# Kernel optimization log

Hardware: AMD Instinct MI355X
Metric: run time of the kernel (lower is better)

The kernel has to match this reference:

```python
import jax, jax.numpy as jnp
import numpy as np

NUM_HEADS = 12

def setup_inputs() -> dict:
    key = jax.random.key(0)
    ks = jax.random.split(key, 6)
    B, N, C, P = 16, 785, 768, 48
    return {
        "x": jax.random.normal(ks[0], (B, N, C), jnp.float32),
        "qkv_w": jax.random.normal(ks[1], (3 * C, C), jnp.float32) * 0.02,
        "pos_emb": jax.random.normal(ks[2], (N, N, P), jnp.float32) * 0.02,
        "pos_proj_w": jax.random.normal(ks[3], (NUM_HEADS, P), jnp.float32) * 0.02,
        "proj_w": jax.random.normal(ks[4], (C, C), jnp.float32) * 0.02,
        "proj_b": jnp.zeros((C,), jnp.float32),
    }

def reference(x, qkv_w, pos_emb, pos_proj_w, proj_w, proj_b):
    B, N, C = x.shape
    H = NUM_HEADS
    hd = C // H
    scale = hd ** -0.5
    # qkv projection: [B,N,3C] -> q,k,v each [B,H,N,hd]
    qkv = (x @ qkv_w.T).reshape(B, N, 3, H, hd)
    qkv = jnp.transpose(qkv, (2, 0, 3, 1, 4))
    q, k, v = qkv[0], qkv[1], qkv[2]
    # learned relative-position bias: [H,N,N]
    pos_score = jnp.einsum('nmp,hp->hnm', pos_emb, pos_proj_w)
    # attention scores: scale applied AFTER adding bias (matches original)
    attn = (jnp.einsum('bhnd,bhmd->bhnm', q, k) + pos_score[None]) * scale
    attn = jax.nn.softmax(attn, axis=-1)
    out = jnp.einsum('bhnm,bhmd->bhnd', attn, v)
    out = jnp.transpose(out, (0, 2, 1, 3)).reshape(B, N, C)
    return out @ proj_w.T + proj_b
```

## Files before the change

kernel.cpp:

```cpp
#include <hip/hip_runtime.h>
#include <hip/hip_fp16.h>

#define B_ 16
#define N_ 785
#define NP 800
#define C_ 768
#define H_ 12
#define HD_ 64
#define P_ 48
#define M_ (B_*N_)
#define MP_ (B_*NP)
#define POSW 832
#define VTW  832
#define SLOG2E 0.1803368801111244f

#define OFF_Q   0
#define OFF_K   9646080
#define OFF_VT  19292160
#define OFF_POS 29515776
#define OFF_XF  37353216
#define OFF_AO  OFF_XF
#define OFF_WQ  47085312
#define OFF_WP  48854784

struct __align__(16) Half8 { __half h[8]; };
typedef _Float16 half8_t __attribute__((ext_vector_type(8)));
typedef _Float16 half4_t __attribute__((ext_vector_type(4)));
typedef float f32x4 __attribute__((ext_vector_type(4)));

__device__ __forceinline__ void gl16(const void* g, void* l) {
    __builtin_amdgcn_global_load_lds(
        (const __attribute__((address_space(1))) void*)g,
        (__attribute__((address_space(3))) void*)l, 16, 0, 0);
}

__device__ __forceinline__ int xcd_swz(int o, int nwg) {
    const int q = nwg >> 3, r = nwg & 7;
    const int xcd = o & 7, idx = o >> 3;
    const int base = xcd < r ? xcd * (q + 1) : r * (q + 1) + (xcd - r) * q;
    return base + idx;
}

#define NX4 2411520
#define NQ4 442368
#define NP4 147456
#define NTOT4 (NX4+NQ4+NP4)

__global__ __launch_bounds__(256) void convert_f16(
    const float* __restrict__ x, const float* __restrict__ wq,
    const float* __restrict__ wp, _Float16* __restrict__ xo,
    _Float16* __restrict__ wqo, _Float16* __restrict__ wpo)
{
    int i = blockIdx.x * 256 + threadIdx.x;
    const float4* s; _Float16* d; int o;
    if (i < NX4)            { s = (const float4*)x;  d = xo;  o = i; }
    else if (i < NX4 + NQ4) { s = (const float4*)wq; d = wqo; o = i - NX4; }
    else                    { s = (const float4*)wp; d = wpo; o = i - NX4 - NQ4; }
    float4 v = s[o];
    half4_t h = { (_Float16)v.x, (_Float16)v.y, (_Float16)v.z, (_Float16)v.w };
    *(half4_t*)&d[o * 4] = h;
}

#define QKV_NWG (18 * 100)

__global__ __launch_bounds__(256) void qkv_gemm_mfma(
    const _Float16* __restrict__ A, const _Float16* __restrict__ Bw,
    _Float16* __restrict__ qh, _Float16* __restrict__ kh, _Float16* __restrict__ vth)
{
    __shared__ _Float16 Asl[2][128 * 32];
    __shared__ _Float16 Bsl[2][128 * 32];

    const int t  = threadIdx.x;
    const int w  = t >> 6;
    const int l  = t & 63;
    const int lr = l & 15;
    const int lg = l >> 4;
    const int wm = (w >> 1) * 64;
    const int wn = (w & 1) * 64;

    const int g   = xcd_swz(blockIdx.x, QKV_NWG);
    const int nt  = g % 18;
    const int n0  = nt * 128;
    const int mp0 = (g / 18) * 128;
    const int tsel  = nt / 6;
    const bool isV  = (tsel == 2);
    const int nbase = n0 - tsel * 768;

    const int f1 = t + 256;
    const int ar0 = t >> 2,  ac0 = (t & 3) * 8;
    const int ar1 = f1 >> 2, ac1 = (f1 & 3) * 8;
    const int mpa = mp0 + ar0, mpb = mp0 + ar1;
    const int xra = (mpa / NP) * N_ + min(mpa % NP, N_ - 1);
    const int xrb = (mpb / NP) * N_ + min(mpb % NP, N_ - 1);
    const _Float16* Ag0 = A  + (size_t)xra * 768 + ac0;
    const _Float16* Ag1 = A  + (size_t)xrb * 768 + ac1;
    const _Float16* Bg0 = Bw + (size_t)(n0 + ar0) * 768 + ac0;
    const _Float16* Bg1 = Bw + (size_t)(n0 + ar1) * 768 + ac1;

    f32x4 acc[4][4];
    #pragma unroll
    for (int i = 0; i < 4; ++i)
        #pragma unroll
        for (int j = 0; j < 4; ++j) acc[i][j] = (f32x4){0.f, 0.f, 0.f, 0.f};

    gl16(Ag0, &Asl[0][t * 8]); gl16(Ag1, &Asl[0][f1 * 8]);
    gl16(Bg0, &Bsl[0][t * 8]); gl16(Bg1, &Bsl[0][f1 * 8]);
    __syncthreads();

    #pragma unroll 2
    for (int it = 0; it < 24; ++it) {
        const int cur = it & 1;
        if (it < 23) {
            const int kn = (it + 1) * 32;
            gl16(Ag0 + kn, &Asl[cur ^ 1][t * 8]); gl16(Ag1 + kn, &Asl[cur ^ 1][f1 * 8]);
            gl16(Bg0 + kn, &Bsl[cur ^ 1][t * 8]); gl16(Bg1 + kn, &Bsl[cur ^ 1][f1 * 8]);
        }
        half8_t af[4], bf[4];
        #pragma unroll
        for (int i = 0; i < 4; ++i)
            af[i] = *(const half8_t*)&Asl[cur][(wm + i * 16 + lr) * 32 + lg * 8];
        #pragma unroll
        for (int j = 0; j < 4; ++j)
            bf[j] = *(const half8_t*)&Bsl[cur][(wn + j * 16 + lr) * 32 + lg * 8];
        __builtin_amdgcn_s_setprio(1);
        if (!isV) {
            #pragma unroll
            for (int i = 0; i < 4; ++i)
                #pragma unroll
                for (int j = 0; j < 4; ++j)
                    acc[i][j] = __builtin_amdgcn_mfma_f32_16x16x32_f16(bf[j], af[i], acc[i][j], 0, 0, 0);
        } else {
            #pragma unroll
            for (int i = 0; i < 4; ++i)
                #pragma unroll
                for (int j = 0; j < 4; ++j)
                    acc[i][j] = __builtin_amdgcn_mfma_f32_16x16x32_f16(af[i], bf[j], acc[i][j], 0, 0, 0);
        }
        __builtin_amdgcn_s_setprio(0);
        __syncthreads();
    }

    if (!isV) {
        _Float16* dstb = (tsel == 0) ? qh : kh;
        const float sc  = (tsel == 0) ? SLOG2E : 1.0f;
        #pragma unroll
        for (int i = 0; i < 4; ++i) {
            const int mp = mp0 + wm + i * 16 + lr;
            const int bb = mp / NP;
            const int nn = mp - bb * NP;
            if (nn >= N_) continue;
            #pragma unroll
            for (int j = 0; j < 4; ++j) {
                const int nq = nbase + wn + j * 16 + lg * 4;
                const int hh = nq >> 6, dd = nq & 63;
                half4_t hv = { (_Float16)(acc[i][j][0] * sc), (_Float16)(acc[i][j][1] * sc),
                               (_Float16)(acc[i][j][2] * sc), (_Float16)(acc[i][j][3] * sc) };
                *(half4_t*)(dstb + ((size_t)(bb * H_ + hh) * N_ + nn) * HD_ + dd) = hv;
            }
        }
    } else {
        #pragma unroll
        for (int i = 0; i < 4; ++i) {
            const int mq  = mp0 + wm + i * 16 + lg * 4;
            const int bb  = mq / NP;
            const int nn0 = mq - bb * NP;
            if (nn0 >= N_) continue;
            const bool full = (nn0 + 3) < N_;
            #pragma unroll
            for (int j = 0; j < 4; ++j) {
                const int n  = nbase + wn + j * 16 + lr;
                const int hh = n >> 6, dd = n & 63;
                _Float16* vb = vth + ((size_t)(bb * H_ + hh) * HD_ + dd) * VTW;
                if (full) {
                    half4_t hv = { (_Float16)acc[i][j][0], (_Float16)acc[i][j][1],
                                   (_Float16)acc[i][j][2], (_Float16)acc[i][j][3] };
                    *(half4_t*)(vb + nn0) = hv;
                } else {
                    #pragma unroll
                    for (int r = 0; r < 4; ++r)
                        if (nn0 + r < N_) vb[nn0 + r] = (_Float16)acc[i][j][r];
                }
            }
        }
    }
}

__global__ __launch_bounds__(256) void pos_kernel(
    const float* __restrict__ pe, const float* __restrict__ pw,
    __half* __restrict__ posh)
{
    __shared__ float W[H_][P_];
    const int t = threadIdx.x;
    for (int i = t; i < H_ * P_; i += 256) W[i / P_][i % P_] = pw[i];
    __syncthreads();
    int nm = blockIdx.x * 256 + t;
    if (nm >= N_ * N_) return;
    float e[48];
    const float4* src = (const float4*)(pe + (size_t)nm * 48);
    #pragma unroll
    for (int i = 0; i < 12; ++i) {
        float4 v = src[i];
        e[4*i] = v.x; e[4*i+1] = v.y; e[4*i+2] = v.z; e[4*i+3] = v.w;
    }
    int n = nm / N_, m = nm - n * N_;
    #pragma unroll
    for (int hh = 0; hh < H_; ++hh) {
        float s = 0.f;
        #pragma unroll
        for (int p = 0; p < 48; ++p) s = fmaf(e[p], W[hh][p], s);
        posh[((size_t)hh * N_ + n) * POSW + m] = __float2half(s * SLOG2E);
    }
}

#define NQT 13
#define ATT_NWG (192 * NQT)

__global__ __launch_bounds__(256) void attn_mfma(
    const _Float16* __restrict__ qh, const _Float16* __restrict__ kh,
    const _Float16* __restrict__ vt, const _Float16* __restrict__ posh,
    _Float16* __restrict__ aoh)
{
    __shared__ _Float16 Kl[2][64][72];
    __shared__ _Float16 Vl[2][64][72];

    const int t  = threadIdx.x;
    const int l  = t & 63;
    const int w  = t >> 6;
    const int lr = l & 15;
    const int lg = l >> 4;

    const int g2   = xcd_swz(blockIdx.x, ATT_NWG);
    const int qt   = g2 % NQT;
    const int rest = g2 / NQT;
    const int b    = rest & 15;
    const int h    = rest >> 4;
    const int bh   = b * H_ + h;
    const int n0   = qt * 64;

    const int qrow = n0 + w * 16 + lr;
    const int qrc  = qrow < N_ ? qrow : N_ - 1;
    const _Float16* qbase = qh + ((size_t)bh * N_ + qrc) * HD_;
    const half8_t qf0 = *(const half8_t*)(qbase + lg * 8);
    const half8_t qf1 = *(const half8_t*)(qbase + 32 + lg * 8);

    f32x4 O0 = {0.f,0.f,0.f,0.f}, O1 = O0, O2 = O0, O3 = O0;
    f32x4 lacc = {0.f,0.f,0.f,0.f};
    float m_run = -1e30f;

    const half8_t vones = { (_Float16)1.f, (_Float16)1.f, (_Float16)1.f, (_Float16)1.f,
                            (_Float16)1.f, (_Float16)1.f, (_Float16)1.f, (_Float16)1.f };

    const int srow = t >> 2;
    const int scol = (t & 3) * 16;
    const int vbase = (scol & 32) + ((scol & 16) >> 2);
    const _Float16* kRow = kh + ((size_t)bh * N_) * HD_ + scol;
    const _Float16* vRow = vt + ((size_t)bh * HD_ + srow) * VTW + scol;
    const _Float16* bFrag = posh + ((size_t)h * N_ + qrc) * POSW + lg * 4;

    half8_t rk0, rk1, rv0, rv1;
    half4_t rbc[4], rbn[4];
    {
        const int gm = srow < N_ ? srow : N_ - 1;
        const half8_t* ks = (const half8_t*)(kRow + (size_t)gm * HD_);
        rk0 = ks[0]; rk1 = ks[1];
        const half8_t* vs = (const half8_t*)vRow;
        rv0 = vs[0]; rv1 = vs[1];
        #pragma unroll
        for (int ms = 0; ms < 4; ++ms)
            rbc[ms] = *(const half4_t*)(bFrag + ms * 16);
    }
    *(half8_t*)&Kl[0][srow][scol]     = rk0;
    *(half8_t*)&Kl[0][srow][scol + 8] = rk1;
    {
        _Float16* vd = &Vl[0][srow][vbase];
        *(half4_t*)(vd +  0) = __builtin_shufflevector(rv0, rv0, 0, 1, 2, 3);
        *(half4_t*)(vd +  8) = __builtin_shufflevector(rv0, rv0, 4, 5, 6, 7);
        *(half4_t*)(vd + 16) = __builtin_shufflevector(rv1, rv1, 0, 1, 2, 3);
        *(half4_t*)(vd + 24) = __builtin_shufflevector(rv1, rv1, 4, 5, 6, 7);
    }

    for (int c = 0; c < 13; ++c) {
        const int cur = c & 1;
        __syncthreads();

        if (c < 12) {
            const int m0n = (c + 1) * 64;
            const int gm  = (m0n + srow) < N_ ? (m0n + srow) : N_ - 1;
            const half8_t* ks = (const half8_t*)(kRow + (size_t)gm * HD_);
            rk0 = ks[0]; rk1 = ks[1];
            const half8_t* vs = (const half8_t*)(vRow + m0n);
            rv0 = vs[0]; rv1 = vs[1];
            #pragma unroll
            for (int ms = 0; ms < 4; ++ms)
                rbn[ms] = *(const half4_t*)(bFrag + m0n + ms * 16);
        }

        f32x4 s[4];
        __builtin_amdgcn_s_setprio(1);
        #pragma unroll
        for (int ms = 0; ms < 4; ++ms) {
            f32x4 acc = { (float)rbc[ms][0], (float)rbc[ms][1],
                          (float)rbc[ms][2], (float)rbc[ms][3] };
            half8_t k0 = *(const half8_t*)&Kl[cur][ms * 16 + lr][lg * 8];
            half8_t k1 = *(const half8_t*)&Kl[cur][ms * 16 + lr][32 + lg * 8];
            acc = __builtin_amdgcn_mfma_f32_16x16x32_f16(k0, qf0, acc, 0, 0, 0);
            acc = __builtin_amdgcn_mfma_f32_16x16x32_f16(k1, qf1, acc, 0, 0, 0);
            s[ms] = acc;
        }
        __builtin_amdgcn_s_setprio(0);

        if (c == 12) {
            #pragma unroll
            for (int ms = 0; ms < 4; ++ms)
                #pragma unroll
                for (int r = 0; r < 4; ++r)
                    if (ms * 16 + lg * 4 + r >= 17) s[ms][r] = -1e30f;
        }

        float x0 = fmaxf(fmaxf(s[0][0], s[0][1]), s[0][2]);
        float x1 = fmaxf(fmaxf(s[0][3], s[1][0]), s[1][1]);
        float x2 = fmaxf(fmaxf(s[1][2], s[1][3]), s[2][0]);
        float x3 = fmaxf(fmaxf(s[2][1], s[2][2]), s[2][3]);
        float x4 = fmaxf(fmaxf(s[3][0], s[3][1]), s[3][2]);
        float mq = fmaxf(fmaxf(fmaxf(x0, x1), x2),
                         fmaxf(fmaxf(x3, x4), s[3][3]));

        if (__any(mq > m_run + 8.f)) {
            float v = fmaxf(mq, __shfl_xor(mq, 16));
            v = fmaxf(v, __shfl_xor(v, 32));
            const float mn    = fmaxf(m_run, v);
            const float alpha = exp2f(m_run - mn);
            m_run = mn;
            const float a0 = __shfl(alpha, lg * 4 + 0);
            const float a1 = __shfl(alpha, lg * 4 + 1);
            const float a2 = __shfl(alpha, lg * 4 + 2);
            const float a3 = __shfl(alpha, lg * 4 + 3);
            O0[0]*=a0; O0[1]*=a1; O0[2]*=a2; O0[3]*=a3;
            O1[0]*=a0; O1[1]*=a1; O1[2]*=a2; O1[3]*=a3;
            O2[0]*=a0; O2[1]*=a1; O2[2]*=a2; O2[3]*=a3;
            O3[0]*=a0; O3[1]*=a1; O3[2]*=a2; O3[3]*=a3;
            lacc[0]*=a0; lacc[1]*=a1; lacc[2]*=a2; lacc[3]*=a3;
        }

        float p[4][4];
        #pragma unroll
        for (int ms = 0; ms < 4; ++ms)
            #pragma unroll
            for (int r = 0; r < 4; ++r)
                p[ms][r] = exp2f(s[ms][r] - m_run);

        half8_t pa0 = { (_Float16)p[0][0], (_Float16)p[0][1], (_Float16)p[0][2], (_Float16)p[0][3],
                        (_Float16)p[1][0], (_Float16)p[1][1], (_Float16)p[1][2], (_Float16)p[1][3] };
        half8_t pa1 = { (_Float16)p[2][0], (_Float16)p[2][1], (_Float16)p[2][2], (_Float16)p[2][3],
                        (_Float16)p[3][0], (_Float16)p[3][1], (_Float16)p[3][2], (_Float16)p[3][3] };

        __builtin_amdgcn_s_setprio(1);
        lacc = __builtin_amdgcn_mfma_f32_16x16x32_f16(pa0, vones, lacc, 0, 0, 0);
        lacc = __builtin_amdgcn_mfma_f32_16x16x32_f16(pa1, vones, lacc, 0, 0, 0);
        #pragma unroll
        for (int ds = 0; ds < 4; ++ds) {
            const _Float16* vr = &Vl[cur][ds * 16 + lr][0];
            half8_t vf0 = *(const half8_t*)&vr[lg * 8];
            half8_t vf1 = *(const half8_t*)&vr[32 + lg * 8];
            f32x4& Od = (ds == 0 ? O0 : ds == 1 ? O1 : ds == 2 ? O2 : O3);
            Od = __builtin_amdgcn_mfma_f32_16x16x32_f16(pa0, vf0, Od, 0, 0, 0);
            Od = __builtin_amdgcn_mfma_f32_16x16x32_f16(pa1, vf1, Od, 0, 0, 0);
        }
        __builtin_amdgcn_s_setprio(0);

        if (c < 12) {
            const int nxt = cur ^ 1;
            *(half8_t*)&Kl[nxt][srow][scol]     = rk0;
            *(half8_t*)&Kl[nxt][srow][scol + 8] = rk1;
            _Float16* vd = &Vl[nxt][srow][vbase];
            *(half4_t*)(vd +  0) = __builtin_shufflevector(rv0, rv0, 0, 1, 2, 3);
            *(half4_t*)(vd +  8) = __builtin_shufflevector(rv0, rv0, 4, 5, 6, 7);
            *(half4_t*)(vd + 16) = __builtin_shufflevector(rv1, rv1, 0, 1, 2, 3);
            *(half4_t*)(vd + 24) = __builtin_shufflevector(rv1, rv1, 4, 5, 6, 7);
            #pragma unroll
            for (int ms = 0; ms < 4; ++ms) rbc[ms] = rbn[ms];
        }
    }

    const int bb = bh / H_;
    #pragma unroll
    for (int r = 0; r < 4; ++r) {
        const int n = n0 + w * 16 + lg * 4 + r;
        if (n >= N_) continue;
        const float inv = 1.f / lacc[r];
        _Float16* dst = aoh + ((size_t)(bb * N_ + n)) * C_ + h * HD_;
        dst[0 * 16 + lr] = (_Float16)(O0[r] * inv);
        dst[1 * 16 + lr] = (_Float16)(O1[r] * inv);
        dst[2 * 16 + lr] = (_Float16)(O2[r] * inv);
        dst[3 * 16 + lr] = (_Float16)(O3[r] * inv);
    }
}

#define PROJ_NWG (6 * 99)

__global__ __launch_bounds__(256) void proj_gemm_mfma(
    const _Float16* __restrict__ A, const _Float16* __restrict__ Bw,
    const float* __restrict__ bias, float* __restrict__ out)
{
    __shared__ _Float16 Asl[2][128 * 32];
    __shared__ _Float16 Bsl[2][128 * 32];

    const int t  = threadIdx.x;
    const int w  = t >> 6;
    const int l  = t & 63;
    const int lr = l & 15;
    const int lg = l >> 4;
    const int wm = (w >> 1) * 64;
    const int wn = (w & 1) * 64;

    const int g  = xcd_swz(blockIdx.x, PROJ_NWG);
    const int n0 = (g % 6) * 128;
    const int m0 = (g / 6) * 128;

    const int f1 = t + 256;
    const int ar0 = t >> 2,  ac0 = (t & 3) * 8;
    const int ar1 = f1 >> 2, ac1 = (f1 & 3) * 8;
    const int ma0 = min(m0 + ar0, M_ - 1);
    const int ma1 = min(m0 + ar1, M_ - 1);
    const _Float16* Ag0 = A  + (size_t)ma0 * 768 + ac0;
    const _Float16* Ag1 = A  + (size_t)ma1 * 768 + ac1;
    const _Float16* Bg0 = Bw + (size_t)(n0 + ar0) * 768 + ac0;
    const _Float16* Bg1 = Bw + (size_t)(n0 + ar1) * 768 + ac1;

    f32x4 acc[4][4];
    #pragma unroll
    for (int i = 0; i < 4; ++i)
        #pragma unroll
        for (int j = 0; j < 4; ++j) acc[i][j] = (f32x4){0.f, 0.f, 0.f, 0.f};

    gl16(Ag0, &Asl[0][t * 8]); gl16(Ag1, &Asl[0][f1 * 8]);
    gl16(Bg0, &Bsl[0][t * 8]); gl16(Bg1, &Bsl[0][f1 * 8]);
    __syncthreads();

    #pragma unroll 2
    for (int it = 0; it < 24; ++it) {
        const int cur = it & 1;
        if (it < 23) {
            const int kn = (it + 1) * 32;
            gl16(Ag0 + kn, &Asl[cur ^ 1][t * 8]); gl16(Ag1 + kn, &Asl[cur ^ 1][f1 * 8]);
            gl16(Bg0 + kn, &Bsl[cur ^ 1][t * 8]); gl16(Bg1 + kn, &Bsl[cur ^ 1][f1 * 8]);
        }
        half8_t af[4], bf[4];
        #pragma unroll
        for (int i = 0; i < 4; ++i)
            af[i] = *(const half8_t*)&Asl[cur][(wm + i * 16 + lr) * 32 + lg * 8];
        #pragma unroll
        for (int j = 0; j < 4; ++j)
            bf[j] = *(const half8_t*)&Bsl[cur][(wn + j * 16 + lr) * 32 + lg * 8];
        __builtin_amdgcn_s_setprio(1);
        #pragma unroll
        for (int i = 0; i < 4; ++i)
            #pragma unroll
            for (int j = 0; j < 4; ++j)
                acc[i][j] = __builtin_amdgcn_mfma_f32_16x16x32_f16(bf[j], af[i], acc[i][j], 0, 0, 0);
        __builtin_amdgcn_s_setprio(0);
        __syncthreads();
    }

    float4 bj4[4];
    #pragma unroll
    for (int j = 0; j < 4; ++j)
        bj4[j] = *(const float4*)&bias[n0 + wn + j * 16 + lg * 4];
    #pragma unroll
    for (int i = 0; i < 4; ++i) {
        const int m = m0 + wm + i * 16 + lr;
        if (m >= M_) continue;
        #pragma unroll
        for (int j = 0; j < 4; ++j) {
            const int nq = n0 + wn + j * 16 + lg * 4;
            float4 o = { acc[i][j][0] + bj4[j].x, acc[i][j][1] + bj4[j].y,
                         acc[i][j][2] + bj4[j].z, acc[i][j][3] + bj4[j].w };
            *(float4*)&out[(size_t)m * 768 + nq] = o;
        }
    }
}

extern "C" void kernel_launch(void* const* d_in, const int* in_sizes, int n_in,
                              void* d_out, int out_size, void* d_ws, size_t ws_size,
                              hipStream_t stream)
{
    const float* x     = (const float*)d_in[0];
    const float* qkv_w = (const float*)d_in[1];
    const float* pe    = (const float*)d_in[2];
    const float* pw    = (const float*)d_in[3];
    const float* pjw   = (const float*)d_in[4];
    const float* pjb   = (const float*)d_in[5];
    float* out = (float*)d_out;

    _Float16* wsh  = (_Float16*)d_ws;
    _Float16* qh   = wsh + OFF_Q;
    _Float16* kh   = wsh + OFF_K;
    _Float16* vth  = wsh + OFF_VT;
    _Float16* posh = wsh + OFF_POS;
    _Float16* xf   = wsh + OFF_XF;
    _Float16* aoh  = wsh + OFF_AO;
    _Float16* wqf  = wsh + OFF_WQ;
    _Float16* wpf  = wsh + OFF_WP;

    convert_f16<<<dim3(NTOT4 / 256), 256, 0, stream>>>(x, qkv_w, pjw, xf, wqf, wpf);
    qkv_gemm_mfma<<<dim3(QKV_NWG), 256, 0, stream>>>(xf, wqf, qh, kh, vth);
    pos_kernel<<<dim3((N_ * N_ + 255) / 256), 256, 0, stream>>>(pe, pw, (__half*)posh);
    attn_mfma<<<dim3(ATT_NWG), 256, 0, stream>>>(qh, kh, vth, posh, aoh);
    proj_gemm_mfma<<<dim3(PROJ_NWG), 256, 0, stream>>>(aoh, wpf, pjb, out);
}
```

Baseline: 261.6 us.

## Load K/V MFMA fragments directly from global memory, drop LDS double buffering

The attention kernel no longer stages K and V tiles through double-buffered shared memory with __syncthreads. Each wave now loads its K and V MFMA operand fragments straight from global memory (relying on L1/L2 for reuse across the 4 waves), and the loop becomes a lambda called per chunk with the last chunk specialised. The running max is also initialised to 0 instead of -1e30. This removes LDS traffic and block barriers, but each wave now issues its own global loads (4x redundant across waves) with no explicit prefetch, so latency hiding relies on occupancy.

```diff
diff --git a/kernel.cpp b/kernel.cpp
--- a/kernel.cpp
+++ b/kernel.cpp
@@ -220,9 +220,6 @@
     const _Float16* __restrict__ vt, const _Float16* __restrict__ posh,
     _Float16* __restrict__ aoh)
 {
-    __shared__ _Float16 Kl[2][64][72];
-    __shared__ _Float16 Vl[2][64][72];
-
     const int t  = threadIdx.x;
     const int l  = t & 63;
     const int w  = t >> 6;
@@ -245,71 +242,55 @@
 
     f32x4 O0 = {0.f,0.f,0.f,0.f}, O1 = O0, O2 = O0, O3 = O0;
     f32x4 lacc = {0.f,0.f,0.f,0.f};
-    float m_run = -1e30f;
+    float m_run = 0.f;
 
     const half8_t vones = { (_Float16)1.f, (_Float16)1.f, (_Float16)1.f, (_Float16)1.f,
                             (_Float16)1.f, (_Float16)1.f, (_Float16)1.f, (_Float16)1.f };
 
-    const int srow = t >> 2;
-    const int scol = (t & 3) * 16;
-    const int vbase = (scol & 32) + ((scol & 16) >> 2);
-    const _Float16* kRow = kh + ((size_t)bh * N_) * HD_ + scol;
-    const _Float16* vRow = vt + ((size_t)bh * HD_ + srow) * VTW + scol;
+    const _Float16* kBase = kh + ((size_t)bh * N_) * HD_ + lg * 8;
+    const _Float16* vB0 = vt + ((size_t)bh * HD_ + (0 * 16 + lr)) * VTW + lg * 4;
+    const _Float16* vB1 = vt + ((size_t)bh * HD_ + (1 * 16 + lr)) * VTW + lg * 4;
+    const _Float16* vB2 = vt + ((size_t)bh * HD_ + (2 * 16 + lr)) * VTW + lg * 4;
+    const _Float16* vB3 = vt + ((size_t)bh * HD_ + (3 * 16 + lr)) * VTW + lg * 4;
     const _Float16* bFrag = posh + ((size_t)h * N_ + qrc) * POSW + lg * 4;
 
-    half8_t rk0, rk1, rv0, rv1;
-    half4_t rbc[4], rbn[4];
-    {
-        const int gm = srow < N_ ? srow : N_ - 1;
-        const half8_t* ks = (const half8_t*)(kRow + (size_t)gm * HD_);
-        rk0 = ks[0]; rk1 = ks[1];
-        const half8_t* vs = (const half8_t*)vRow;
-        rv0 = vs[0]; rv1 = vs[1];
+    auto chunk = [&](const int m0, const bool last) {
+        half8_t kf0[4], kf1[4];
+        #pragma unroll
+        for (int ms = 0; ms < 4; ++ms) {
+            int kr = m0 + ms * 16 + lr;
+            if (last) kr = min(kr, N_ - 1);
+            const _Float16* kp = kBase + (size_t)kr * HD_;
+            kf0[ms] = *(const half8_t*)kp;
+            kf1[ms] = *(const half8_t*)(kp + 32);
+        }
+        half4_t v4[4][4];
+        const _Float16* vps[4] = { vB0 + m0, vB1 + m0, vB2 + m0, vB3 + m0 };
+        #pragma unroll
+        for (int ds = 0; ds < 4; ++ds) {
+            v4[ds][0] = *(const half4_t*)(vps[ds]);
+            v4[ds][1] = *(const half4_t*)(vps[ds] + 16);
+            v4[ds][2] = *(const half4_t*)(vps[ds] + 32);
+            v4[ds][3] = *(const half4_t*)(vps[ds] + 48);
+        }
+        half4_t bb[4];
         #pragma unroll
         for (int ms = 0; ms < 4; ++ms)
-            rbc[ms] = *(const half4_t*)(bFrag + ms * 16);
-    }
-    *(half8_t*)&Kl[0][srow][scol]     = rk0;
-    *(half8_t*)&Kl[0][srow][scol + 8] = rk1;
-    {
-        _Float16* vd = &Vl[0][srow][vbase];
-        *(half4_t*)(vd +  0) = __builtin_shufflevector(rv0, rv0, 0, 1, 2, 3);
-        *(half4_t*)(vd +  8) = __builtin_shufflevector(rv0, rv0, 4, 5, 6, 7);
-        *(half4_t*)(vd + 16) = __builtin_shufflevector(rv1, rv1, 0, 1, 2, 3);
-        *(half4_t*)(vd + 24) = __builtin_shufflevector(rv1, rv1, 4, 5, 6, 7);
-    }
-
-    for (int c = 0; c < 13; ++c) {
-        const int cur = c & 1;
-        __syncthreads();
-
-        if (c < 12) {
-            const int m0n = (c + 1) * 64;
-            const int gm  = (m0n + srow) < N_ ? (m0n + srow) : N_ - 1;
-            const half8_t* ks = (const half8_t*)(kRow + (size_t)gm * HD_);
-            rk0 = ks[0]; rk1 = ks[1];
-            const half8_t* vs = (const half8_t*)(vRow + m0n);
-            rv0 = vs[0]; rv1 = vs[1];
-            #pragma unroll
-            for (int ms = 0; ms < 4; ++ms)
-                rbn[ms] = *(const half4_t*)(bFrag + m0n + ms * 16);
-        }
+            bb[ms] = *(const half4_t*)(bFrag + m0 + ms * 16);
 
         f32x4 s[4];
         __builtin_amdgcn_s_setprio(1);
         #pragma unroll
         for (int ms = 0; ms < 4; ++ms) {
-            f32x4 acc = { (float)rbc[ms][0], (float)rbc[ms][1],
-                          (float)rbc[ms][2], (float)rbc[ms][3] };
-            half8_t k0 = *(const half8_t*)&Kl[cur][ms * 16 + lr][lg * 8];
-            half8_t k1 = *(const half8_t*)&Kl[cur][ms * 16 + lr][32 + lg * 8];
-            acc = __builtin_amdgcn_mfma_f32_16x16x32_f16(k0, qf0, acc, 0, 0, 0);
-            acc = __builtin_amdgcn_mfma_f32_16x16x32_f16(k1, qf1, acc, 0, 0, 0);
+            f32x4 acc = { (float)bb[ms][0], (float)bb[ms][1],
+                          (float)bb[ms][2], (float)bb[ms][3] };
+            acc = __builtin_amdgcn_mfma_f32_16x16x32_f16(kf0[ms], qf0, acc, 0, 0, 0);
+            acc = __builtin_amdgcn_mfma_f32_16x16x32_f16(kf1[ms], qf1, acc, 0, 0, 0);
             s[ms] = acc;
         }
         __builtin_amdgcn_s_setprio(0);
 
-        if (c == 12) {
+        if (last) {
             #pragma unroll
             for (int ms = 0; ms < 4; ++ms)
                 #pragma unroll
@@ -359,28 +340,17 @@
         lacc = __builtin_amdgcn_mfma_f32_16x16x32_f16(pa1, vones, lacc, 0, 0, 0);
         #pragma unroll
         for (int ds = 0; ds < 4; ++ds) {
-            const _Float16* vr = &Vl[cur][ds * 16 + lr][0];
-            half8_t vf0 = *(const half8_t*)&vr[lg * 8];
-            half8_t vf1 = *(const half8_t*)&vr[32 + lg * 8];
+            half8_t vf0 = __builtin_shufflevector(v4[ds][0], v4[ds][1], 0, 1, 2, 3, 4, 5, 6, 7);
+            half8_t vf1 = __builtin_shufflevector(v4[ds][2], v4[ds][3], 0, 1, 2, 3, 4, 5, 6, 7);
             f32x4& Od = (ds == 0 ? O0 : ds == 1 ? O1 : ds == 2 ? O2 : O3);
             Od = __builtin_amdgcn_mfma_f32_16x16x32_f16(pa0, vf0, Od, 0, 0, 0);
             Od = __builtin_amdgcn_mfma_f32_16x16x32_f16(pa1, vf1, Od, 0, 0, 0);
         }
         __builtin_amdgcn_s_setprio(0);
-
-        if (c < 12) {
-            const int nxt = cur ^ 1;
-            *(half8_t*)&Kl[nxt][srow][scol]     = rk0;
-            *(half8_t*)&Kl[nxt][srow][scol + 8] = rk1;
-            _Float16* vd = &Vl[nxt][srow][vbase];
-            *(half4_t*)(vd +  0) = __builtin_shufflevector(rv0, rv0, 0, 1, 2, 3);
-            *(half4_t*)(vd +  8) = __builtin_shufflevector(rv0, rv0, 4, 5, 6, 7);
-            *(half4_t*)(vd + 16) = __builtin_shufflevector(rv1, rv1, 0, 1, 2, 3);
-            *(half4_t*)(vd + 24) = __builtin_shufflevector(rv1, rv1, 4, 5, 6, 7);
-            #pragma unroll
-            for (int ms = 0; ms < 4; ++ms) rbc[ms] = rbn[ms];
-        }
-    }
+    };
+
+    for (int c = 0; c < 12; ++c) chunk(c * 64, false);
+    chunk(768, true);
 
     const int bb = bh / H_;
     #pragma unroll
```

Measured after the change: 563.8 us. +115.5%, slower.
